# Kernel optimization log

Measured on AMD Instinct MI355X. Metric: run time of the kernel, lower is better.

The kernel has to match this reference:

```python
import jax, jax.numpy as jnp
import numpy as np

NH = 8       # num_heads
EDIM = 256   # embedding_dim (also per-head dim in this module)
BS, SQL = 4, 1024


def setup_inputs() -> dict:
    key = jax.random.key(0)
    ks = jax.random.split(key, 5)
    scale_in = 1.0 / np.sqrt(EDIM)
    scale_out = 1.0 / np.sqrt(NH * EDIM)
    return {
        "x": jax.random.normal(ks[0], (BS, SQL, EDIM), dtype=jnp.float32),
        "w_attn": jax.random.normal(ks[1], (NH * 3 * EDIM, EDIM), dtype=jnp.float32) * scale_in,
        "b_attn": jax.random.normal(ks[2], (NH * 3 * EDIM,), dtype=jnp.float32) * scale_in,
        "w_out": jax.random.normal(ks[3], (EDIM, NH * EDIM), dtype=jnp.float32) * scale_out,
        "b_out": jax.random.normal(ks[4], (EDIM,), dtype=jnp.float32) * scale_out,
    }


def reference(x, w_attn, b_attn, w_out, b_out):
    bs, sql, edim = x.shape
    nh = NH
    # projections: (bs, sql, nh*3*edim); split into Q, K, V chunks of nh*edim
    proj = x @ w_attn.T + b_attn
    q, k, v = jnp.split(proj, 3, axis=-1)
    # Faithful to torch: raw view (bs, sql, nh*edim) -> (bs, nh, sql, edim),
    # a reinterpretation of memory, NOT a transpose.
    q = q.reshape(bs, nh, sql, edim)
    k = k.reshape(bs, nh, sql, edim)
    v = v.reshape(bs, nh, sql, edim)
    # scaled dot-product scores: (bs, nh, sql, sql)
    scores = jnp.einsum("bhqd,bhkd->bhqk", q, k) / jnp.sqrt(jnp.float32(edim))
    # causal mask: -inf strictly above the diagonal (equivalent to adding triu(-inf, 1))
    causal = jnp.tril(jnp.ones((sql, sql), dtype=bool))
    scores = jnp.where(causal, scores, -jnp.inf)
    attn = jax.nn.softmax(scores, axis=-1)
    out = jnp.einsum("bhqk,bhkd->bhqd", attn, v)
    # Faithful raw view back: (bs, nh, sql, edim) -> (bs, sql, nh*edim)
    out = out.reshape(bs, sql, nh * edim)
    return out @ w_out.T + b_out
```

## Files before the change

### kernel.cpp

```cpp
#include <hip/hip_runtime.h>

#define SQL  1024
#define EDIM 256
#define NHD  8
#define NKV  (NHD * 3 * EDIM)
#define MROWS (4 * SQL)

typedef short bf16x8 __attribute__((ext_vector_type(8)));
typedef float f32x4 __attribute__((ext_vector_type(4)));

__device__ __forceinline__ unsigned short f2bf(float f) {
  unsigned u = __float_as_uint(f);
  u += 0x7fff + ((u >> 16) & 1);
  return (unsigned short)(u >> 16);
}

__device__ __forceinline__ void g2lds16(const void* g, void* l) {
  __builtin_amdgcn_global_load_lds(
      (const __attribute__((address_space(1))) unsigned int*)g,
      (__attribute__((address_space(3))) unsigned int*)l, 16, 0, 0);
}

__device__ __forceinline__ void storev(float* p, float v) { *p = v; }
__device__ __forceinline__ void storev(unsigned short* p, float v) { *p = f2bf(v); }

__global__ __launch_bounds__(256) void cast_bf16(
    const float* __restrict__ in, unsigned short* __restrict__ out, int n8) {
  int i = blockIdx.x * 256 + threadIdx.x;
  if (i >= n8) return;
  float4 a = ((const float4*)in)[2 * i];
  float4 b = ((const float4*)in)[2 * i + 1];
  union { unsigned short s[8]; ulonglong2 v; } u;
  u.s[0] = f2bf(a.x); u.s[1] = f2bf(a.y); u.s[2] = f2bf(a.z); u.s[3] = f2bf(a.w);
  u.s[4] = f2bf(b.x); u.s[5] = f2bf(b.y); u.s[6] = f2bf(b.z); u.s[7] = f2bf(b.w);
  ((ulonglong2*)out)[i] = u.v;
}

template <int BM, int BN, typename OutT>
__global__ __launch_bounds__(256) void gemm_mfma(
    const unsigned short* __restrict__ A, const unsigned short* __restrict__ B,
    const float* __restrict__ bias, OutT* __restrict__ C,
    int M, int N, int K) {
  constexpr int TM = BM / 32, TN = BN / 32;
  __shared__ __align__(16) unsigned short As[2][BM * 32];
  __shared__ __align__(16) unsigned short Bs[2][BN * 32];
  const int tid = threadIdx.x;
  const int wave = tid >> 6, lane = tid & 63;
  const int quad = lane >> 4, l16 = lane & 15;
  const int wm = (wave >> 1) * (BM / 2), wn = (wave & 1) * (BN / 2);
  const int m0 = blockIdx.x * BM, n0 = blockIdx.y * BN;
  const int sw = (l16 >> 1) & 3;

  f32x4 acc[TM][TN];
  #pragma unroll
  for (int i = 0; i < TM; i++)
    #pragma unroll
    for (int j = 0; j < TN; j++) acc[i][j] = {0.f, 0.f, 0.f, 0.f};

  auto stage = [&](int k0, int bb) {
    #pragma unroll
    for (int it = 0; it < BM / 64; it++) {
      int flat = it * 256 + tid;
      int row = flat >> 2;
      int cg = (flat & 3) ^ ((row >> 1) & 3);
      g2lds16(A + (size_t)(m0 + row) * K + k0 + cg * 8, &As[bb][flat * 8]);
    }
    #pragma unroll
    for (int it = 0; it < BN / 64; it++) {
      int flat = it * 256 + tid;
      int row = flat >> 2;
      int cg = (flat & 3) ^ ((row >> 1) & 3);
      g2lds16(B + (size_t)(n0 + row) * K + k0 + cg * 8, &Bs[bb][flat * 8]);
    }
  };

  stage(0, 0);
  __syncthreads();
  for (int k0 = 0; k0 < K; k0 += 32) {
    const int bb = (k0 >> 5) & 1;
    if (k0 + 32 < K) stage(k0 + 32, bb ^ 1);
    bf16x8 af[TM], bf[TN];
    #pragma unroll
    for (int i = 0; i < TM; i++)
      af[i] = *(const bf16x8*)&As[bb][(wm + i * 16 + l16) * 32 + (quad ^ sw) * 8];
    #pragma unroll
    for (int j = 0; j < TN; j++)
      bf[j] = *(const bf16x8*)&Bs[bb][(wn + j * 16 + l16) * 32 + (quad ^ sw) * 8];
    #pragma unroll
    for (int i = 0; i < TM; i++)
      #pragma unroll
      for (int j = 0; j < TN; j++)
        acc[i][j] = __builtin_amdgcn_mfma_f32_16x16x32_bf16(af[i], bf[j], acc[i][j], 0, 0, 0);
    __syncthreads();
  }

  #pragma unroll
  for (int i = 0; i < TM; i++) {
    #pragma unroll
    for (int r = 0; r < 4; r++) {
      int m = m0 + wm + i * 16 + quad * 4 + r;
      #pragma unroll
      for (int j = 0; j < TN; j++) {
        int n = n0 + wn + j * 16 + l16;
        storev(&C[(size_t)m * N + n], acc[i][j][r] + bias[n]);
      }
    }
  }
}

__global__ __launch_bounds__(256) void transpose_v(
    const unsigned short* __restrict__ proj, unsigned short* __restrict__ vt) {
  __shared__ unsigned short T[64][66];
  const int tid = threadIdx.x;
  const int s0 = blockIdx.x * 64, d0 = blockIdx.y * 64, bh = blockIdx.z;
  const int b = bh >> 3, h = bh & 7;
  #pragma unroll
  for (int it = 0; it < 2; it++) {
    int c = it * 256 + tid;
    int sr = c >> 3, k8 = (c & 7) * 8;
    int s = s0 + sr;
    const unsigned short* src = proj + (size_t)(b * SQL + h * 128 + (s >> 3)) * NKV
                                + 2 * 2048 + (s & 7) * 256 + d0 + k8;
    *(ulonglong2*)&T[sr][k8] = *(const ulonglong2*)src;
  }
  __syncthreads();
  #pragma unroll
  for (int it = 0; it < 2; it++) {
    int c = it * 256 + tid;
    int dr = c >> 3, s8 = (c & 7) * 8;
    unsigned short tmp[8];
    #pragma unroll
    for (int j = 0; j < 8; j++) tmp[j] = T[s8 + j][dr];
    unsigned short* dst = vt + ((size_t)bh * EDIM + d0 + dr) * SQL + s0 + s8;
    *(ulonglong2*)dst = *(ulonglong2*)tmp;
  }
}

__global__ __launch_bounds__(256) void attn_mfma(
    const unsigned short* __restrict__ proj,
    const unsigned short* __restrict__ vt,
    unsigned short* __restrict__ oflat) {
  __shared__ __align__(16) unsigned short lds[35328];
  unsigned short* Ps = lds + 32768;

  const int tid = threadIdx.x;
  const int wave = tid >> 6, lane = tid & 63;
  const int quad = lane >> 4, l16 = lane & 15;
  const int slot = blockIdx.x & 255, round = blockIdx.x >> 8;
  const int bh = slot & 31;
  const int j = slot >> 5;
  const int qt = round ? j : 15 - j;
  const int b = bh >> 3, h = bh & 7;
  const int q0 = qt * 64;

  #pragma unroll
  for (int it = 0; it < 8; it++) {
    int c = it * 256 + tid;
    int r = c >> 5, ch = (c & 31) ^ (r & 7);
    int s = q0 + r;
    g2lds16(proj + (size_t)(b * SQL + h * 128 + (s >> 3)) * NKV + (s & 7) * 256 + ch * 8,
            lds + c * 8);
  }
  __syncthreads();
  bf16x8 aq[8];
  const int qrow = wave * 16 + l16;
  #pragma unroll
  for (int kk = 0; kk < 8; kk++)
    aq[kk] = *(const bf16x8*)&lds[qrow * 256 + ((kk * 4 + quad) ^ (qrow & 7)) * 8];
  __syncthreads();

  f32x4 o[16];
  #pragma unroll
  for (int t = 0; t < 16; t++) o[t] = {0.f, 0.f, 0.f, 0.f};
  float l_r[4] = {0.f, 0.f, 0.f, 0.f};

  auto stage = [&](int kt, int bb) {
    unsigned short* KsB = lds + bb * 16384;
    unsigned short* VtB = KsB + 8192;
    #pragma unroll
    for (int it = 0; it < 4; it++) {
      int c = it * 256 + tid;
      int r = c >> 5, ch = (c & 31) ^ (r & 7);
      int s = kt * 32 + r;
      g2lds16(proj + (size_t)(b * SQL + h * 128 + (s >> 3)) * NKV + 2048 + (s & 7) * 256 + ch * 8,
              KsB + c * 8);
    }
    #pragma unroll
    for (int it = 0; it < 4; it++) {
      int c = it * 256 + tid;
      int d = c >> 2, ch = (c & 3) ^ (d & 3);
      g2lds16(vt + ((size_t)bh * EDIM + d) * SQL + kt * 32 + ch * 8, VtB + c * 8);
    }
  };

  const int nkt = 2 * qt + 2;
  stage(0, 0);
  __syncthreads();

  for (int kt = 0; kt < nkt; kt++) {
    const int bb = kt & 1;
    if (kt + 1 < nkt) stage(kt + 1, bb ^ 1);
    const unsigned short* KsB = lds + bb * 16384;
    const unsigned short* VtB = KsB + 8192;

    f32x4 s0 = {0.f, 0.f, 0.f, 0.f}, s1 = {0.f, 0.f, 0.f, 0.f};
    #pragma unroll
    for (int kk = 0; kk < 8; kk++) {
      int ch = (kk * 4 + quad) ^ (l16 & 7);
      bf16x8 b0 = *(const bf16x8*)&KsB[l16 * 256 + ch * 8];
      bf16x8 b1 = *(const bf16x8*)&KsB[(16 + l16) * 256 + ch * 8];
      s0 = __builtin_amdgcn_mfma_f32_16x16x32_bf16(aq[kk], b0, s0, 0, 0, 0);
      s1 = __builtin_amdgcn_mfma_f32_16x16x32_bf16(aq[kk], b1, s1, 0, 0, 0);
    }

    const int kg0 = kt * 32 + l16, kg1 = kg0 + 16;
    #pragma unroll
    for (int r = 0; r < 4; r++) {
      int qg = q0 + wave * 16 + quad * 4 + r;
      float p0 = (kg0 <= qg) ? __expf(s0[r] * 0.0625f) : 0.f;
      float p1 = (kg1 <= qg) ? __expf(s1[r] * 0.0625f) : 0.f;
      l_r[r] += p0 + p1;
      Ps[(wave * 16 + quad * 4 + r) * 40 + l16]      = f2bf(p0);
      Ps[(wave * 16 + quad * 4 + r) * 40 + 16 + l16] = f2bf(p1);
    }

    bf16x8 ap = *(const bf16x8*)&Ps[(wave * 16 + l16) * 40 + quad * 8];
    #pragma unroll
    for (int t = 0; t < 16; t++) {
      bf16x8 bv = *(const bf16x8*)&VtB[(t * 16 + l16) * 32 + (quad ^ (l16 & 3)) * 8];
      o[t] = __builtin_amdgcn_mfma_f32_16x16x32_bf16(ap, bv, o[t], 0, 0, 0);
    }
    __syncthreads();
  }

  #pragma unroll
  for (int r = 0; r < 4; r++) {
    float l = l_r[r];
    #pragma unroll
    for (int off = 1; off < 16; off <<= 1) l += __shfl_xor(l, off);
    float inv = 1.0f / l;
    int s = q0 + wave * 16 + quad * 4 + r;
    unsigned short* dst = oflat + (size_t)(b * SQL + h * 128 + (s >> 3)) * 2048 + (s & 7) * 256;
    #pragma unroll
    for (int t = 0; t < 16; t++)
      dst[t * 16 + l16] = f2bf(o[t][r] * inv);
  }
}

extern "C" void kernel_launch(void* const* d_in, const int* in_sizes, int n_in,
                              void* d_out, int out_size, void* d_ws, size_t ws_size,
                              hipStream_t stream) {
  const float* x      = (const float*)d_in[0];
  const float* w_attn = (const float*)d_in[1];
  const float* b_attn = (const float*)d_in[2];
  const float* w_out  = (const float*)d_in[3];
  const float* b_out  = (const float*)d_in[4];
  float* out = (float*)d_out;

  char* p = (char*)d_ws;
  unsigned short* proj = (unsigned short*)p;  p += (size_t)MROWS * NKV * 2;
  unsigned short* obf  = (unsigned short*)p;  p += (size_t)MROWS * 2048 * 2;
  unsigned short* vtb  = (unsigned short*)p;  p += (size_t)32 * EDIM * SQL * 2;
  unsigned short* xb   = (unsigned short*)p;  p += (size_t)MROWS * EDIM * 2;
  unsigned short* wb   = (unsigned short*)p;  p += (size_t)NKV * EDIM * 2;
  unsigned short* wob  = (unsigned short*)p;

  cast_bf16<<<(MROWS * EDIM / 8 + 255) / 256, 256, 0, stream>>>(x, xb, MROWS * EDIM / 8);
  cast_bf16<<<(NKV * EDIM / 8 + 255) / 256, 256, 0, stream>>>(w_attn, wb, NKV * EDIM / 8);
  cast_bf16<<<(EDIM * 2048 / 8 + 255) / 256, 256, 0, stream>>>(w_out, wob, EDIM * 2048 / 8);

  gemm_mfma<128, 128, unsigned short><<<dim3(MROWS / 128, NKV / 128), 256, 0, stream>>>(
      xb, wb, b_attn, proj, MROWS, NKV, EDIM);
  transpose_v<<<dim3(SQL / 64, EDIM / 64, 32), 256, 0, stream>>>(proj, vtb);
  attn_mfma<<<512, 256, 0, stream>>>(proj, vtb, obf);
  gemm_mfma<64, 64, float><<<dim3(MROWS / 64, EDIM / 64), 256, 0, stream>>>(
      obf, wob, b_out, out, MROWS, EDIM, NHD * EDIM);
}
```

Baseline: 171.0 us.

## Enlarge attention tiles to 128 queries and 64 keys per block

The attention kernel now processes 128 query rows per block, with each wave handling two 16-row subtiles, and stages 64-key K/V tiles into a larger double-buffered LDS region. Each K and V fragment read from LDS is reused by two MFMAs, which cuts LDS and global traffic per flop. The grid drops from 512 to 256 blocks, and the block mapping and per-wave P buffers change to match. Launch bounds and LDS use now allow only one block per CU, so latency hiding is lower. The heavy-first ordering of query tiles is lost, which leaves load imbalance across the causal triangle.

After: 191.7 us. 1.12x slower.

```diff
diff --git a/kernel.cpp b/kernel.cpp
--- a/kernel.cpp
+++ b/kernel.cpp
@@ -136,64 +136,62 @@
   }
 }
 
-__global__ __launch_bounds__(256) void attn_mfma(
+__global__ __launch_bounds__(256, 1) void attn_mfma(
     const unsigned short* __restrict__ proj,
     const unsigned short* __restrict__ vt,
     unsigned short* __restrict__ oflat) {
-  __shared__ __align__(16) unsigned short lds[35328];
-  unsigned short* Ps = lds + 32768;
+  __shared__ __align__(16) unsigned short lds[74752];
 
   const int tid = threadIdx.x;
   const int wave = tid >> 6, lane = tid & 63;
   const int quad = lane >> 4, l16 = lane & 15;
-  const int slot = blockIdx.x & 255, round = blockIdx.x >> 8;
-  const int bh = slot & 31;
-  const int j = slot >> 5;
-  const int qt = round ? j : 15 - j;
+  const int g = blockIdx.x;
+  const int bh = (g & 7) * 4 + ((g >> 3) & 3);
+  const int qt = g >> 5;
   const int b = bh >> 3, h = bh & 7;
-  const int q0 = qt * 64;
-
-  #pragma unroll
-  for (int it = 0; it < 8; it++) {
-    int c = it * 256 + tid;
-    int r = c >> 5, ch = (c & 31) ^ (r & 7);
-    int s = q0 + r;
-    g2lds16(proj + (size_t)(b * SQL + h * 128 + (s >> 3)) * NKV + (s & 7) * 256 + ch * 8,
-            lds + c * 8);
-  }
-  __syncthreads();
-  bf16x8 aq[8];
-  const int qrow = wave * 16 + l16;
-  #pragma unroll
-  for (int kk = 0; kk < 8; kk++)
-    aq[kk] = *(const bf16x8*)&lds[qrow * 256 + ((kk * 4 + quad) ^ (qrow & 7)) * 8];
-  __syncthreads();
-
-  f32x4 o[16];
-  #pragma unroll
-  for (int t = 0; t < 16; t++) o[t] = {0.f, 0.f, 0.f, 0.f};
-  float l_r[4] = {0.f, 0.f, 0.f, 0.f};
+  const int q0 = qt * 128;
+  unsigned short* Ps = lds + 65536 + wave * 2304;
+
+  bf16x8 aq[2][8];
+  #pragma unroll
+  for (int st = 0; st < 2; st++) {
+    int s = q0 + wave * 32 + st * 16 + l16;
+    const unsigned short* qrow =
+        proj + (size_t)(b * SQL + h * 128 + (s >> 3)) * NKV + (s & 7) * 256;
+    #pragma unroll
+    for (int kk = 0; kk < 8; kk++)
+      aq[st][kk] = *(const bf16x8*)(qrow + kk * 32 + quad * 8);
+  }
 
   auto stage = [&](int kt, int bb) {
     unsigned short* KsB = lds + bb * 16384;
-    unsigned short* VtB = KsB + 8192;
-    #pragma unroll
-    for (int it = 0; it < 4; it++) {
-      int c = it * 256 + tid;
-      int r = c >> 5, ch = (c & 31) ^ (r & 7);
-      int s = kt * 32 + r;
-      g2lds16(proj + (size_t)(b * SQL + h * 128 + (s >> 3)) * NKV + 2048 + (s & 7) * 256 + ch * 8,
-              KsB + c * 8);
-    }
-    #pragma unroll
-    for (int it = 0; it < 4; it++) {
-      int c = it * 256 + tid;
-      int d = c >> 2, ch = (c & 3) ^ (d & 3);
-      g2lds16(vt + ((size_t)bh * EDIM + d) * SQL + kt * 32 + ch * 8, VtB + c * 8);
+    unsigned short* VtB = lds + 32768 + bb * 16384;
+    #pragma unroll
+    for (int it = 0; it < 8; it++) {
+      int flat = it * 256 + tid;
+      int row = flat >> 5, ch = (flat & 31) ^ (row & 7);
+      int s = kt * 64 + row;
+      g2lds16(proj + (size_t)(b * SQL + h * 128 + (s >> 3)) * NKV + 2048
+                   + (s & 7) * 256 + ch * 8,
+              KsB + flat * 8);
+    }
+    #pragma unroll
+    for (int it = 0; it < 8; it++) {
+      int flat = it * 256 + tid;
+      int d = flat >> 3, ch = (flat & 7) ^ (d & 7);
+      g2lds16(vt + ((size_t)bh * EDIM + d) * SQL + kt * 64 + ch * 8,
+              VtB + flat * 8);
     }
   };
 
-  const int nkt = 2 * qt + 2;
+  f32x4 o[2][16];
+  #pragma unroll
+  for (int st = 0; st < 2; st++)
+    #pragma unroll
+    for (int t = 0; t < 16; t++) o[st][t] = {0.f, 0.f, 0.f, 0.f};
+  float l_r[2][4] = {};
+
+  const int nkt = 2 * (qt + 1);
   stage(0, 0);
   __syncthreads();
 
@@ -201,49 +199,69 @@
     const int bb = kt & 1;
     if (kt + 1 < nkt) stage(kt + 1, bb ^ 1);
     const unsigned short* KsB = lds + bb * 16384;
-    const unsigned short* VtB = KsB + 8192;
-
-    f32x4 s0 = {0.f, 0.f, 0.f, 0.f}, s1 = {0.f, 0.f, 0.f, 0.f};
-    #pragma unroll
-    for (int kk = 0; kk < 8; kk++) {
-      int ch = (kk * 4 + quad) ^ (l16 & 7);
-      bf16x8 b0 = *(const bf16x8*)&KsB[l16 * 256 + ch * 8];
-      bf16x8 b1 = *(const bf16x8*)&KsB[(16 + l16) * 256 + ch * 8];
-      s0 = __builtin_amdgcn_mfma_f32_16x16x32_bf16(aq[kk], b0, s0, 0, 0, 0);
-      s1 = __builtin_amdgcn_mfma_f32_16x16x32_bf16(aq[kk], b1, s1, 0, 0, 0);
-    }
-
-    const int kg0 = kt * 32 + l16, kg1 = kg0 + 16;
+    const unsigned short* VtB = lds + 32768 + bb * 16384;
+
+    f32x4 s[2][4];
+    #pragma unroll
+    for (int st = 0; st < 2; st++)
+      #pragma unroll
+      for (int c = 0; c < 4; c++) s[st][c] = {0.f, 0.f, 0.f, 0.f};
+    #pragma unroll
+    for (int c = 0; c < 4; c++) {
+      #pragma unroll
+      for (int kk = 0; kk < 8; kk++) {
+        int ch = (kk * 4 + quad) ^ (l16 & 7);
+        bf16x8 bk = *(const bf16x8*)&KsB[(c * 16 + l16) * 256 + ch * 8];
+        s[0][c] = __builtin_amdgcn_mfma_f32_16x16x32_bf16(aq[0][kk], bk, s[0][c], 0, 0, 0);
+        s[1][c] = __builtin_amdgcn_mfma_f32_16x16x32_bf16(aq[1][kk], bk, s[1][c], 0, 0, 0);
+      }
+    }
+
+    #pragma unroll
+    for (int st = 0; st < 2; st++) {
+      #pragma unroll
+      for (int c = 0; c < 4; c++) {
+        int kg = kt * 64 + c * 16 + l16;
+        #pragma unroll
+        for (int r = 0; r < 4; r++) {
+          int qg = q0 + wave * 32 + st * 16 + quad * 4 + r;
+          float p = (kg <= qg) ? __expf(s[st][c][r] * 0.0625f) : 0.f;
+          l_r[st][r] += p;
+          Ps[(st * 16 + quad * 4 + r) * 72 + c * 16 + l16] = f2bf(p);
+        }
+      }
+    }
+
+    #pragma unroll
+    for (int kc = 0; kc < 2; kc++) {
+      bf16x8 ap0 = *(const bf16x8*)&Ps[l16 * 72 + (kc * 4 + quad) * 8];
+      bf16x8 ap1 = *(const bf16x8*)&Ps[(16 + l16) * 72 + (kc * 4 + quad) * 8];
+      #pragma unroll
+      for (int t = 0; t < 16; t++) {
+        int ch = (kc * 4 + quad) ^ (l16 & 7);
+        bf16x8 bv = *(const bf16x8*)&VtB[(t * 16 + l16) * 64 + ch * 8];
+        o[0][t] = __builtin_amdgcn_mfma_f32_16x16x32_bf16(ap0, bv, o[0][t], 0, 0, 0);
+        o[1][t] = __builtin_amdgcn_mfma_f32_16x16x32_bf16(ap1, bv, o[1][t], 0, 0, 0);
+      }
+    }
+    __syncthreads();
+  }
+
+  #pragma unroll
+  for (int st = 0; st < 2; st++) {
     #pragma unroll
     for (int r = 0; r < 4; r++) {
-      int qg = q0 + wave * 16 + quad * 4 + r;
-      float p0 = (kg0 <= qg) ? __expf(s0[r] * 0.0625f) : 0.f;
-      float p1 = (kg1 <= qg) ? __expf(s1[r] * 0.0625f) : 0.f;
-      l_r[r] += p0 + p1;
-      Ps[(wave * 16 + quad * 4 + r) * 40 + l16]      = f2bf(p0);
-      Ps[(wave * 16 + quad * 4 + r) * 40 + 16 + l16] = f2bf(p1);
-    }
-
-    bf16x8 ap = *(const bf16x8*)&Ps[(wave * 16 + l16) * 40 + quad * 8];
-    #pragma unroll
-    for (int t = 0; t < 16; t++) {
-      bf16x8 bv = *(const bf16x8*)&VtB[(t * 16 + l16) * 32 + (quad ^ (l16 & 3)) * 8];
-      o[t] = __builtin_amdgcn_mfma_f32_16x16x32_bf16(ap, bv, o[t], 0, 0, 0);
-    }
-    __syncthreads();
-  }
-
-  #pragma unroll
-  for (int r = 0; r < 4; r++) {
-    float l = l_r[r];
-    #pragma unroll
-    for (int off = 1; off < 16; off <<= 1) l += __shfl_xor(l, off);
-    float inv = 1.0f / l;
-    int s = q0 + wave * 16 + quad * 4 + r;
-    unsigned short* dst = oflat + (size_t)(b * SQL + h * 128 + (s >> 3)) * 2048 + (s & 7) * 256;
-    #pragma unroll
-    for (int t = 0; t < 16; t++)
-      dst[t * 16 + l16] = f2bf(o[t][r] * inv);
+      float l = l_r[st][r];
+      #pragma unroll
+      for (int off = 1; off < 16; off <<= 1) l += __shfl_xor(l, off);
+      float inv = 1.0f / l;
+      int s = q0 + wave * 32 + st * 16 + quad * 4 + r;
+      unsigned short* dst =
+          oflat + (size_t)(b * SQL + h * 128 + (s >> 3)) * 2048 + (s & 7) * 256;
+      #pragma unroll
+      for (int t = 0; t < 16; t++)
+        dst[t * 16 + l16] = f2bf(o[st][t][r] * inv);
+    }
   }
 }
 
@@ -272,7 +290,7 @@
   gemm_mfma<128, 128, unsigned short><<<dim3(MROWS / 128, NKV / 128), 256, 0, stream>>>(
       xb, wb, b_attn, proj, MROWS, NKV, EDIM);
   transpose_v<<<dim3(SQL / 64, EDIM / 64, 32), 256, 0, stream>>>(proj, vtb);
-  attn_mfma<<<512, 256, 0, stream>>>(proj, vtb, obf);
+  attn_mfma<<<256, 256, 0, stream>>>(proj, vtb, obf);
   gemm_mfma<64, 64, float><<<dim3(MROWS / 64, EDIM / 64), 256, 0, stream>>>(
       obf, wob, b_out, out, MROWS, EDIM, NHD * EDIM);
 }
```
